# Kernel optimization log

Hardware: AMD Instinct MI355X
Metric: run time of the kernel (lower is better)

Reference implementation:

```python
import jax, jax.numpy as jnp
import numpy as np

N, E, F_IN, HID, G = 20000, 320000, 128, 128, 64
H, D = 8, 32  # TransformerConv heads, per-head dim


def setup_inputs() -> dict:
    key = jax.random.key(0)
    ks = jax.random.split(key, 24)
    def w(k, i, o):
        return (jax.random.normal(k, (i, o), jnp.float32) / np.float32(np.sqrt(i)))
    def b(k, o):
        return jax.random.normal(k, (o,), jnp.float32) * 0.01
    inp = {
        'x': jax.random.normal(ks[0], (N, F_IN), jnp.float32),
        'edge_index': jax.random.randint(ks[1], (2, E), 0, N, jnp.int32),
        'batch': jnp.sort(jax.random.randint(ks[2], (N,), 0, G, jnp.int32)),
        # SAGEConv 1: 128 -> 128 (lin_l has bias, lin_r none)
        's1_wl': w(ks[3], 128, 128), 's1_bl': b(ks[4], 128), 's1_wr': w(ks[5], 128, 128),
        # SAGEConv 2: 128 -> 256
        's2_wl': w(ks[6], 128, 256), 's2_bl': b(ks[7], 256), 's2_wr': w(ks[8], 128, 256),
        # TransformerConv 1: 256 -> 8*32
        't1_wq': w(ks[9], 256, 256), 't1_bq': b(ks[10], 256),
        't1_wk': w(ks[11], 256, 256), 't1_bk': b(ks[12], 256),
        't1_wv': w(ks[13], 256, 256), 't1_bv': b(ks[14], 256),
        't1_ws': w(ks[15], 256, 256), 't1_bs': b(ks[16], 256),
        # TransformerConv 2
        't2_wq': w(ks[17], 256, 256), 't2_bq': b(ks[18], 256),
        't2_wk': w(ks[19], 256, 256), 't2_bk': b(ks[20], 256),
        't2_wv': w(ks[21], 256, 256), 't2_bv': b(ks[22], 256),
        't2_ws': w(ks[23], 256, 256), 't2_bs': b(jax.random.fold_in(key, 100), 256),
        # proj MLP: 256 -> 512 -> HID
        'p1_w': w(jax.random.fold_in(key, 101), 256, 512), 'p1_b': b(jax.random.fold_in(key, 102), 512),
        'p2_w': w(jax.random.fold_in(key, 103), 512, HID), 'p2_b': b(jax.random.fold_in(key, 104), HID),
    }
    return inp


def _sage(x, src, dst, wl, bl, wr):
    # PyG SAGEConv (aggr='mean'): lin_l(mean_j x_j) + lin_r(x_i)
    s = jax.ops.segment_sum(x[src], dst, num_segments=N)           # [N,F]
    cnt = jax.ops.segment_sum(jnp.ones((src.shape[0], 1), x.dtype), dst, num_segments=N)
    mean = s / jnp.maximum(cnt, 1.0)
    return mean @ wl + bl + x @ wr


def _tconv(x, src, dst, wq, bq, wk, bk, wv, bv, ws, bs):
    # PyG TransformerConv(256, 32, heads=8): per-edge attention + skip
    q = (x @ wq + bq).reshape(N, H, D)
    k = (x @ wk + bk).reshape(N, H, D)
    v = (x @ wv + bv).reshape(N, H, D)
    logits = jnp.einsum('ehd,ehd->eh', q[dst], k[src]) / np.float32(np.sqrt(D))  # [E,H]
    m = jax.ops.segment_max(logits, dst, num_segments=N)           # [N,H]
    p = jnp.exp(logits - m[dst])
    denom = jax.ops.segment_sum(p, dst, num_segments=N)
    p = p / denom[dst]                                              # softmax per target node per head
    agg = jax.ops.segment_sum(p[:, :, None] * v[src], dst, num_segments=N)  # [N,H,D]
    return agg.reshape(N, H * D) + x @ ws + bs


def reference(x, edge_index, batch, s1_wl, s1_bl, s1_wr, s2_wl, s2_bl, s2_wr,
              t1_wq, t1_bq, t1_wk, t1_bk, t1_wv, t1_bv, t1_ws, t1_bs,
              t2_wq, t2_bq, t2_wk, t2_bk, t2_wv, t2_bv, t2_ws, t2_bs,
              p1_w, p1_b, p2_w, p2_b):
    src, dst = edge_index[0], edge_index[1]
    h = jax.nn.relu(_sage(x, src, dst, s1_wl, s1_bl, s1_wr))
    h = jax.nn.relu(_sage(h, src, dst, s2_wl, s2_bl, s2_wr))
    h = jax.nn.relu(_tconv(h, src, dst, t1_wq, t1_bq, t1_wk, t1_bk, t1_wv, t1_bv, t1_ws, t1_bs))
    h = jax.nn.relu(_tconv(h, src, dst, t2_wq, t2_bq, t2_wk, t2_bk, t2_wv, t2_bv, t2_ws, t2_bs))
    # proj: ReLU -> Linear(256,512) -> ReLU -> Linear(512,HID) -> Sigmoid
    h = jax.nn.relu(h)
    h = jax.nn.relu(h @ p1_w + p1_b)
    h = jax.nn.sigmoid(h @ p2_w + p2_b)
    return jax.ops.segment_max(h, batch, num_segments=G)            # global_max_pool [G,HID]
```

## Files before the change

### kernel.cpp

```cpp
#include <hip/hip_runtime.h>
#include <hip/hip_bf16.h>
#include <hip/hip_fp16.h>
#include <math.h>

#define NN 20000
#define EE 320000
#define GG 64
#define CH 16

typedef __hip_bfloat16 bf16;
typedef __attribute__((ext_vector_type(8))) short short8;
typedef __attribute__((ext_vector_type(4))) float f32x4;
typedef __attribute__((ext_vector_type(4))) uint uint4v;
typedef __attribute__((ext_vector_type(2))) _Float16 half2v;
typedef unsigned int uint;
typedef unsigned short ushort;

__device__ __forceinline__ float bfr2f(ushort u) {
    union { uint i; float f; } c; c.i = ((uint)u) << 16; return c.f;
}
__device__ __forceinline__ ushort f2bfr(float f) {
    bf16 h = __float2bfloat16(f);
    return *(ushort*)&h;
}

__device__ __forceinline__ float dot2acc(uint a, uint b, float c) {
#if __has_builtin(__builtin_amdgcn_fdot2)
    return __builtin_amdgcn_fdot2(__builtin_bit_cast(half2v, a),
                                  __builtin_bit_cast(half2v, b), c, false);
#else
    half2v ha = __builtin_bit_cast(half2v, a);
    half2v hb = __builtin_bit_cast(half2v, b);
    return c + (float)ha.x * (float)hb.x + (float)ha.y * (float)hb.y;
#endif
}

__device__ __forceinline__ void load_lds16(const void* g, void* l) {
    __builtin_amdgcn_global_load_lds(
        (const __attribute__((address_space(1))) unsigned int*)g,
        (__attribute__((address_space(3))) unsigned int*)l, 16, 0, 0);
}

template <int KW, int NW, int KTOT, int KOFF>
__device__ __forceinline__ void tpose(int local, const float* __restrict__ W,
                                      bf16* __restrict__ Wt) {
    constexpr int SH = (KW == 128) ? 7 : ((KW == 256) ? 8 : 9);
    int n = local >> SH;
    int k = local & (KW - 1);
    Wt[(size_t)n * KTOT + KOFF + k] = __float2bfloat16(W[(size_t)k * NW + n]);
}

#define PREP_CONV  10000
#define PREP_PACK  (PREP_CONV + 3200)
#define PREP_BIAS  (PREP_PACK + 8)
#define PREP_COUNT (PREP_BIAS + 1250)

__global__ __launch_bounds__(256) void prep_kernel(
    const float* x, bf16* xm1,
    const float* s1_wr, const float* s1_wl, const float* s2_wr, const float* s2_wl,
    const float* t1_wq, const float* t1_wk, const float* t1_wv, const float* t1_ws,
    const float* t2_wq, const float* t2_wk, const float* t2_wv, const float* t2_ws,
    const float* p1_w, const float* p2_w,
    bf16* w1cat, bf16* w2cat, bf16* qw1, bf16* qw2, bf16* p1t, bf16* p2t,
    const float* b1q, const float* b1k, const float* b1v, const float* b1s,
    const float* b2q, const float* b2k, const float* b2v, const float* b2s,
    float* qb1, float* qb2,
    const int* dst, int* cnt) {
    int bid = blockIdx.x;
    int tid = threadIdx.x;
    if (bid < PREP_CONV) {
        int i = bid * 256 + tid;
        int r = i >> 7, c = i & 127;
        xm1[(size_t)r * 256 + c] = __float2bfloat16(x[i]);
    } else if (bid < PREP_PACK) {
        int i = (bid - PREP_CONV) * 256 + tid;
        if (i < 16384)        tpose<128, 128, 256, 0>(i, s1_wr, w1cat);
        else if (i < 32768)   tpose<128, 128, 256, 128>(i - 16384, s1_wl, w1cat);
        else if (i < 65536)   tpose<128, 256, 256, 0>(i - 32768, s2_wr, w2cat);
        else if (i < 98304)   tpose<128, 256, 256, 128>(i - 65536, s2_wl, w2cat);
        else if (i < 163840)  tpose<256, 256, 256, 0>(i - 98304,  t1_wq, qw1);
        else if (i < 229376)  tpose<256, 256, 256, 0>(i - 163840, t1_wk, qw1 + 65536);
        else if (i < 294912)  tpose<256, 256, 256, 0>(i - 229376, t1_wv, qw1 + 131072);
        else if (i < 360448)  tpose<256, 256, 256, 0>(i - 294912, t1_ws, qw1 + 196608);
        else if (i < 425984)  tpose<256, 256, 256, 0>(i - 360448, t2_wq, qw2);
        else if (i < 491520)  tpose<256, 256, 256, 0>(i - 425984, t2_wk, qw2 + 65536);
        else if (i < 557056)  tpose<256, 256, 256, 0>(i - 491520, t2_wv, qw2 + 131072);
        else if (i < 622592)  tpose<256, 256, 256, 0>(i - 557056, t2_ws, qw2 + 196608);
        else if (i < 753664)  tpose<256, 512, 256, 0>(i - 622592, p1_w, p1t);
        else if (i < 819200)  tpose<512, 128, 512, 0>(i - 753664, p2_w, p2t);
    } else if (bid < PREP_BIAS) {
        int i = (bid - PREP_PACK) * 256 + tid;
        if (i < 2048) {
            float* d = (i < 1024) ? qb1 : qb2;
            int j = i & 1023;
            const float* s;
            if (i < 1024) s = (j < 256) ? b1q : (j < 512) ? b1k : (j < 768) ? b1v : b1s;
            else          s = (j < 256) ? b2q : (j < 512) ? b2k : (j < 768) ? b2v : b2s;
            d[j] = s[j & 255];
        }
    } else {
        int e = (bid - PREP_BIAS) * 256 + tid;
        if (e < EE) atomicAdd(&cnt[dst[e]], 1);
    }
}

__global__ __launch_bounds__(1024) void scan_kernel(int* __restrict__ cnt,
                                                    int* __restrict__ off, int n) {
    __shared__ int wsum[16];
    __shared__ int carry_s;
    int tid = threadIdx.x;
    int lane = tid & 63, wid = tid >> 6;
    if (tid == 0) { carry_s = 0; off[0] = 0; }
    __syncthreads();
    for (int base = 0; base < n; base += 1024) {
        int idx = base + tid;
        int val = (idx < n) ? cnt[idx] : 0;
        int x = val;
        #pragma unroll
        for (int s = 1; s < 64; s <<= 1) {
            int y = __shfl_up(x, s, 64);
            if (lane >= s) x += y;
        }
        if (lane == 63) wsum[wid] = x;
        __syncthreads();
        if (tid == 0) {
            int c = carry_s;
            #pragma unroll
            for (int w = 0; w < 16; w++) { int t = wsum[w]; wsum[w] = c; c += t; }
            carry_s = c;
        }
        __syncthreads();
        int incl = wsum[wid] + x;
        if (idx < n) {
            off[idx + 1] = incl;
            cnt[idx] = incl - val;
        }
        __syncthreads();
    }
}

__global__ __launch_bounds__(256) void fill_kernel(const int* __restrict__ src,
                                                   const int* __restrict__ dst,
                                                   int* __restrict__ cursor,
                                                   int* __restrict__ csr_src, int E) {
    int e = blockIdx.x * 256 + threadIdx.x;
    if (e < E) {
        int p = atomicAdd(&cursor[dst[e]], 1);
        csr_src[p] = src[e];
    }
}

__global__ __launch_bounds__(256) void mean2_kernel(const bf16* __restrict__ x, int xstride,
                                                    const int* __restrict__ off,
                                                    const int* __restrict__ csr_src,
                                                    bf16* __restrict__ outp, int ostride) {
    int node = blockIdx.x * 4 + (threadIdx.x >> 6);
    int lane = threadIdx.x & 63;
    int e0 = off[node], e1 = off[node + 1];
    float s0 = 0.f, s1 = 0.f;
    int e = e0;
    for (; e + 7 < e1; e += 8) {
        uint a[8];
        #pragma unroll
        for (int j = 0; j < 8; j++) {
            int sa = csr_src[e + j];
            a[j] = *(const uint*)(x + (size_t)sa * xstride + lane * 2);
        }
        #pragma unroll
        for (int j = 0; j < 8; j++) {
            union { uint i; float f; } t;
            t.i = a[j] << 16; s0 += t.f;
            t.i = a[j] & 0xffff0000u; s1 += t.f;
        }
    }
    for (; e < e1; e++) {
        int sa = csr_src[e];
        uint a = *(const uint*)(x + (size_t)sa * xstride + lane * 2);
        union { uint i; float f; } t;
        t.i = a << 16; s0 += t.f; t.i = a & 0xffff0000u; s1 += t.f;
    }
    int deg = e1 - e0;
    float inv = (deg > 0) ? 1.f / (float)deg : 0.f;
    uint r = ((uint)f2bfr(s1 * inv) << 16) | (uint)f2bfr(s0 * inv);
    *(uint*)(outp + (size_t)node * ostride + lane * 2) = r;
}

template <int MODE, int TM>
__global__ __launch_bounds__(256, (TM == 128) ? 3 : 4)
void gemm_kernel(const bf16* __restrict__ A,
                 const bf16* __restrict__ Wt,
                 const float* __restrict__ bias,
                 void* __restrict__ Cv,
                 int M, int K, int N, int cstride,
                 const int* __restrict__ batch,
                 float* __restrict__ pool_out) {
    constexpr int NT = (TM == 128) ? 4 : 2;
    __shared__ short As[TM * 64];
    __shared__ short Bs[128 * 64];
    __shared__ int bat[TM];
    int t = threadIdx.x;
    int lane = t & 63;
    int wave = t >> 6;
    int wm = (TM == 128) ? (wave >> 1) * 64 : 0;
    int wn = (TM == 128) ? (wave & 1) * 64 : wave * 32;
    int bm = blockIdx.y * TM, bn = blockIdx.x * 128;
    int quad = lane >> 4, l16 = lane & 15;
    int srow = t >> 3;
    int scol = (t & 7) * 8;

    if (MODE == 4 && t < TM) bat[t] = batch[min(bm + t, M - 1)];

    f32x4 acc[4][NT];
    f32x4 zero = {0.f, 0.f, 0.f, 0.f};
    #pragma unroll
    for (int i = 0; i < 4; i++)
        #pragma unroll
        for (int j = 0; j < NT; j++) acc[i][j] = zero;

    for (int kk = 0; kk < K; kk += 64) {
        #pragma unroll
        for (int r = 0; r < TM / 32; r++) {
            int row = r * 32 + srow;
            int gm = bm + row; gm = (gm < M) ? gm : (M - 1);
            load_lds16(A + (size_t)gm * K + kk + scol, &As[row * 64 + scol]);
        }
        #pragma unroll
        for (int r = 0; r < 4; r++) {
            int row = r * 32 + srow;
            load_lds16(Wt + (size_t)(bn + row) * K + kk + scol, &Bs[row * 64 + scol]);
        }
        __syncthreads();
        #pragma unroll
        for (int ks = 0; ks < 2; ks++) {
            short8 af[4], bfr[NT];
            #pragma unroll
            for (int i = 0; i < 4; i++)
                af[i] = *(const short8*)&As[(wm + i * 16 + l16) * 64 + ks * 32 + quad * 8];
            #pragma unroll
            for (int j = 0; j < NT; j++)
                bfr[j] = *(const short8*)&Bs[(wn + j * 16 + l16) * 64 + ks * 32 + quad * 8];
            #pragma unroll
            for (int i = 0; i < 4; i++)
                #pragma unroll
                for (int j = 0; j < NT; j++)
                    acc[i][j] = __builtin_amdgcn_mfma_f32_16x16x32_bf16(af[i], bfr[j], acc[i][j], 0, 0, 0);
        }
        __syncthreads();
    }

    if (MODE == 4) {
        int g0 = bat[0], gL = bat[TM - 1];
        #pragma unroll
        for (int j = 0; j < NT; j++) {
            int gn = bn + wn + j * 16 + l16;
            float m0 = 0.f, m1 = 0.f;
            #pragma unroll
            for (int i = 0; i < 4; i++) {
                #pragma unroll
                for (int r = 0; r < 4; r++) {
                    int row = i * 16 + quad * 4 + r;
                    int gm = bm + row;
                    if (gm >= M) continue;
                    float v = acc[i][j][r] + bias[gn];
                    v = 1.f / (1.f + expf(-v));
                    int g = bat[row];
                    if (g == g0) m0 = fmaxf(m0, v);
                    else if (g == gL) m1 = fmaxf(m1, v);
                    else atomicMax((int*)&pool_out[g * 128 + gn], __float_as_int(v));
                }
            }
            m0 = fmaxf(m0, __shfl_xor(m0, 16));
            m0 = fmaxf(m0, __shfl_xor(m0, 32));
            m1 = fmaxf(m1, __shfl_xor(m1, 16));
            m1 = fmaxf(m1, __shfl_xor(m1, 32));
            if (quad == 0) {
                atomicMax((int*)&pool_out[g0 * 128 + gn], __float_as_int(m0));
                if (gL != g0)
                    atomicMax((int*)&pool_out[gL * 128 + gn], __float_as_int(m1));
            }
        }
        return;
    }

    #pragma unroll
    for (int i = 0; i < 4; i++) {
        int gm0 = bm + wm + i * 16 + quad * 4;
        #pragma unroll
        for (int j = 0; j < NT; j++) {
            int gn = bn + wn + j * 16 + l16;
            #pragma unroll
            for (int r = 0; r < 4; r++) {
                int gm = gm0 + r;
                if (gm >= M) continue;
                float v = acc[i][j][r] + bias[gn];
                if (MODE == 2) v = fmaxf(v, 0.f);
                ushort st;
                if (MODE == 5 && gn < 512) {
                    __half hh = __float2half(v);
                    st = *(ushort*)&hh;
                } else {
                    st = f2bfr(v);
                }
                ((ushort*)Cv)[(size_t)gm * cstride + gn] = st;
            }
        }
    }
}

template <int MODE, int TM>
static void launch_gemm(const bf16* A, const bf16* Wt, const float* bias, void* C,
                        int M, int K, int N, int cstride, hipStream_t st,
                        const int* batch = nullptr, float* pool_out = nullptr) {
    dim3 grid(N / 128, (M + TM - 1) / TM);
    hipLaunchKernelGGL((gemm_kernel<MODE, TM>), grid, dim3(256), 0, st,
                       A, Wt, bias, C, M, K, N, cstride, batch, pool_out);
}

__global__ __launch_bounds__(256) void attn5_kernel(const bf16* __restrict__ qkvs,
                                                    const int* __restrict__ off,
                                                    const int* __restrict__ csr_src,
                                                    bf16* __restrict__ out, int ostride) {
    __shared__ float pp[2][CH][9];
    __shared__ int srcs[2][CH];
    int i = blockIdx.x;
    int tid = threadIdx.x;
    int ea = tid >> 4, ha = (tid >> 1) & 7, half = tid & 1;
    int hc = tid >> 5, dp = (tid >> 1) & 15, epar = tid & 1;

    uint q2[8];
    {
        const uint4v* qp = (const uint4v*)(qkvs + (size_t)i * 1024 + ha * 32 + half * 16);
        uint4v a = qp[0], b = qp[1];
        q2[0] = a.x; q2[1] = a.y; q2[2] = a.z; q2[3] = a.w;
        q2[4] = b.x; q2[5] = b.y; q2[6] = b.z; q2[7] = b.w;
    }

    int e0 = off[i], e1 = off[i + 1];
    float l = 0.f, acc0 = 0.f, acc1 = 0.f;
    int vcol = 512 + hc * 32 + dp * 2;
    if (e0 < e1) {
        if (tid < CH) srcs[0][tid] = csr_src[min(e0 + tid, e1 - 1)];
        __syncthreads();
        int buf = 0;
        for (int base = e0; base < e1; base += CH, buf ^= 1) {
            int cnt = min(CH, e1 - base);
            uint vv[8];
            #pragma unroll
            for (int j = 0; j < 8; j++) {
                int e = epar + j * 2;
                vv[j] = *(const uint*)(qkvs + (size_t)srcs[buf][e] * 1024 + vcol);
            }
            int s = srcs[buf][ea];
            const uint4v* kp = (const uint4v*)(qkvs + (size_t)s * 1024 + 256 + ha * 32 + half * 16);
            uint4v ka = kp[0], kb = kp[1];
            if (tid < CH) srcs[buf ^ 1][tid] = csr_src[min(base + CH + tid, e1 - 1)];
            float d = 0.f;
            d = dot2acc(q2[0], ka.x, d); d = dot2acc(q2[1], ka.y, d);
            d = dot2acc(q2[2], ka.z, d); d = dot2acc(q2[3], ka.w, d);
            d = dot2acc(q2[4], kb.x, d); d = dot2acc(q2[5], kb.y, d);
            d = dot2acc(q2[6], kb.z, d); d = dot2acc(q2[7], kb.w, d);
            d += __shfl_xor(d, 1);
            float p = (ea < cnt) ? __expf(d * 0.17677669529663687f) : 0.f;
            if (half == 0) pp[buf][ea][ha] = p;
            __syncthreads();
            #pragma unroll
            for (int j = 0; j < 8; j++) {
                int e = epar + j * 2;
                float pj = pp[buf][e][hc];
                l += pj;
                union { uint i; float f; } lo, hi;
                lo.i = vv[j] << 16; hi.i = vv[j] & 0xffff0000u;
                acc0 += pj * lo.f;
                acc1 += pj * hi.f;
            }
        }
    }
    acc0 += __shfl_xor(acc0, 1);
    acc1 += __shfl_xor(acc1, 1);
    l    += __shfl_xor(l, 1);
    float inv = (l > 0.f) ? 1.f / l : 0.f;
    float r0 = acc0 * inv, r1 = acc1 * inv;
    if (epar == 0) {
        uint su = *(const uint*)(qkvs + (size_t)i * 1024 + 768 + hc * 32 + dp * 2);
        union { uint i; float f; } lo, hi;
        lo.i = su << 16; hi.i = su & 0xffff0000u;
        float v0 = fmaxf(r0 + lo.f, 0.f);
        float v1 = fmaxf(r1 + hi.f, 0.f);
        uint packed = ((uint)f2bfr(v1) << 16) | (uint)f2bfr(v0);
        *(uint*)(out + (size_t)i * ostride + hc * 32 + dp * 2) = packed;
    }
}

extern "C" void kernel_launch(void* const* d_in, const int* in_sizes, int n_in,
                              void* d_out, int out_size, void* d_ws, size_t ws_size,
                              hipStream_t stream) {
    const float* x      = (const float*)d_in[0];
    const int*   ei     = (const int*)d_in[1];
    const int*   batch  = (const int*)d_in[2];
    const float* s1_wl  = (const float*)d_in[3];
    const float* s1_bl  = (const float*)d_in[4];
    const float* s1_wr  = (const float*)d_in[5];
    const float* s2_wl  = (const float*)d_in[6];
    const float* s2_bl  = (const float*)d_in[7];
    const float* s2_wr  = (const float*)d_in[8];
    const float* t1_wq  = (const float*)d_in[9];
    const float* t1_bq  = (const float*)d_in[10];
    const float* t1_wk  = (const float*)d_in[11];
    const float* t1_bk  = (const float*)d_in[12];
    const float* t1_wv  = (const float*)d_in[13];
    const float* t1_bv  = (const float*)d_in[14];
    const float* t1_ws  = (const float*)d_in[15];
    const float* t1_bs  = (const float*)d_in[16];
    const float* t2_wq  = (const float*)d_in[17];
    const float* t2_bq  = (const float*)d_in[18];
    const float* t2_wk  = (const float*)d_in[19];
    const float* t2_bk  = (const float*)d_in[20];
    const float* t2_wv  = (const float*)d_in[21];
    const float* t2_bv  = (const float*)d_in[22];
    const float* t2_wsk = (const float*)d_in[23];
    const float* t2_bs  = (const float*)d_in[24];
    const float* p1_w   = (const float*)d_in[25];
    const float* p1_b   = (const float*)d_in[26];
    const float* p2_w   = (const float*)d_in[27];
    const float* p2_b   = (const float*)d_in[28];
    float* out = (float*)d_out;

    char* ws = (char*)d_ws;
    size_t o = 0;
    auto alloc = [&](size_t bytes) { char* p = ws + o; o += (bytes + 255) & ~(size_t)255; return p; };
    int* off     = (int*)alloc(sizeof(int) * (NN + 1));
    int* cursor  = (int*)alloc(sizeof(int) * NN);
    int* csr_src = (int*)alloc(sizeof(int) * EE);
    bf16* w1cat = (bf16*)alloc(2 * 128 * 256);
    bf16* w2cat = (bf16*)alloc(2 * 256 * 256);
    bf16* qw1   = (bf16*)alloc(2 * 1024 * 256);
    bf16* qw2   = (bf16*)alloc(2 * 1024 * 256);
    bf16* p1t   = (bf16*)alloc(2 * 512 * 256);
    bf16* p2t   = (bf16*)alloc(2 * 128 * 512);
    float* qb1  = (float*)alloc(4 * 1024);
    float* qb2  = (float*)alloc(4 * 1024);
    bf16* xm1   = (bf16*)alloc(2 * (size_t)NN * 256);
    bf16* xm2   = (bf16*)alloc(2 * (size_t)NN * 256);
    bf16* t1b   = (bf16*)alloc(2 * (size_t)NN * 512);
    bf16* Q     = (bf16*)alloc(2 * (size_t)NN * 1024);
    bf16* h2   = xm1;
    bf16* t1   = t1b;
    bf16* h4   = xm1;
    bf16* p1o  = t1b;

    const int* src = ei;
    const int* dst = ei + EE;

    hipMemsetAsync(cursor, 0, sizeof(int) * NN, stream);
    hipMemsetAsync(out, 0, sizeof(float) * (size_t)out_size, stream);

    prep_kernel<<<PREP_COUNT, 256, 0, stream>>>(
        x, xm1,
        s1_wr, s1_wl, s2_wr, s2_wl,
        t1_wq, t1_wk, t1_wv, t1_ws,
        t2_wq, t2_wk, t2_wv, t2_wsk,
        p1_w, p2_w,
        w1cat, w2cat, qw1, qw2, p1t, p2t,
        t1_bq, t1_bk, t1_bv, t1_bs,
        t2_bq, t2_bk, t2_bv, t2_bs,
        qb1, qb2,
        dst, cursor);

    scan_kernel<<<1, 1024, 0, stream>>>(cursor, off, NN);
    fill_kernel<<<(EE + 255) / 256, 256, 0, stream>>>(src, dst, cursor, csr_src, EE);

    mean2_kernel<<<NN / 4, 256, 0, stream>>>(xm1, 256, off, csr_src, xm1 + 128, 256);
    launch_gemm<2, 64>(xm1, w1cat, s1_bl, xm2, NN, 256, 128, 256, stream);

    mean2_kernel<<<NN / 4, 256, 0, stream>>>(xm2, 256, off, csr_src, xm2 + 128, 256);
    launch_gemm<2, 64>(xm2, w2cat, s2_bl, h2, NN, 256, 256, 256, stream);

    launch_gemm<5, 128>(h2, qw1, qb1, Q, NN, 256, 1024, 1024, stream);
    attn5_kernel<<<NN, 256, 0, stream>>>(Q, off, csr_src, t1, 256);

    launch_gemm<5, 128>(t1, qw2, qb2, Q, NN, 256, 1024, 1024, stream);
    attn5_kernel<<<NN, 256, 0, stream>>>(Q, off, csr_src, h4, 256);

    launch_gemm<2, 128>(h4, p1t, p1_b, p1o, NN, 256, 512, 512, stream);
    launch_gemm<4, 64>(p1o, p2t, p2_b, nullptr, NN, 512, 128, 128, stream, batch, out);
}
```

Baseline: 437.5 us.

## Map one wavefront per node in attention and drop shared-memory syncs

```diff
diff --git a/kernel.cpp b/kernel.cpp
--- a/kernel.cpp
+++ b/kernel.cpp
@@ -6,12 +6,12 @@
 #define NN 20000
 #define EE 320000
 #define GG 64
-#define CH 16
 
 typedef __hip_bfloat16 bf16;
 typedef __attribute__((ext_vector_type(8))) short short8;
 typedef __attribute__((ext_vector_type(4))) float f32x4;
-typedef __attribute__((ext_vector_type(4))) uint uint4v;
+typedef __attribute__((ext_vector_type(4))) unsigned int uint4v;
+typedef __attribute__((ext_vector_type(2))) unsigned int uint2v;
 typedef __attribute__((ext_vector_type(2))) _Float16 half2v;
 typedef unsigned int uint;
 typedef unsigned short ushort;
@@ -316,79 +316,76 @@
                        A, Wt, bias, C, M, K, N, cstride, batch, pool_out);
 }
 
-__global__ __launch_bounds__(256) void attn5_kernel(const bf16* __restrict__ qkvs,
-                                                    const int* __restrict__ off,
-                                                    const int* __restrict__ csr_src,
-                                                    bf16* __restrict__ out, int ostride) {
-    __shared__ float pp[2][CH][9];
-    __shared__ int srcs[2][CH];
-    int i = blockIdx.x;
+__global__ __launch_bounds__(256, 8) void attn6_kernel(const bf16* __restrict__ qkvs,
+                                                       const int* __restrict__ off,
+                                                       const int* __restrict__ csr_src,
+                                                       bf16* __restrict__ out, int ostride) {
     int tid = threadIdx.x;
-    int ea = tid >> 4, ha = (tid >> 1) & 7, half = tid & 1;
-    int hc = tid >> 5, dp = (tid >> 1) & 15, epar = tid & 1;
-
-    uint q2[8];
-    {
-        const uint4v* qp = (const uint4v*)(qkvs + (size_t)i * 1024 + ha * 32 + half * 16);
-        uint4v a = qp[0], b = qp[1];
-        q2[0] = a.x; q2[1] = a.y; q2[2] = a.z; q2[3] = a.w;
-        q2[4] = b.x; q2[5] = b.y; q2[6] = b.z; q2[7] = b.w;
-    }
-
-    int e0 = off[i], e1 = off[i + 1];
-    float l = 0.f, acc0 = 0.f, acc1 = 0.f;
-    int vcol = 512 + hc * 32 + dp * 2;
+    int node = blockIdx.x * 4 + (tid >> 6);
+    int l = tid & 63;
+    int g = l >> 4;
+    int lg = l & 15;
+    int h = l >> 3;
+
+    const bf16* row_i = qkvs + (size_t)node * 1024;
+    uint4v qa = *(const uint4v*)(row_i + lg * 16);
+    uint4v qb = *(const uint4v*)(row_i + lg * 16 + 8);
+
+    int e0 = off[node], e1 = off[node + 1];
+    float acc0 = 0.f, acc1 = 0.f, acc2 = 0.f, acc3 = 0.f, lsum = 0.f;
+
     if (e0 < e1) {
-        if (tid < CH) srcs[0][tid] = csr_src[min(e0 + tid, e1 - 1)];
-        __syncthreads();
-        int buf = 0;
-        for (int base = e0; base < e1; base += CH, buf ^= 1) {
-            int cnt = min(CH, e1 - base);
-            uint vv[8];
-            #pragma unroll
-            for (int j = 0; j < 8; j++) {
-                int e = epar + j * 2;
-                vv[j] = *(const uint*)(qkvs + (size_t)srcs[buf][e] * 1024 + vcol);
+        int sc[4];
+        #pragma unroll
+        for (int e = 0; e < 4; e++) sc[e] = csr_src[min(e0 + e, e1 - 1)];
+        for (int base = e0; base < e1; base += 4) {
+            int cnt = e1 - base;
+            int sn[4];
+            #pragma unroll
+            for (int e = 0; e < 4; e++) sn[e] = csr_src[min(base + 4 + e, e1 - 1)];
+            const bf16* krow = qkvs + (size_t)sc[g] * 1024 + 256 + lg * 16;
+            uint4v ka = *(const uint4v*)(krow);
+            uint4v kb = *(const uint4v*)(krow + 8);
+            uint2v vv[4];
+            #pragma unroll
+            for (int e = 0; e < 4; e++)
+                vv[e] = *(const uint2v*)(qkvs + (size_t)sc[e] * 1024 + 512 + 4 * l);
+            float d = 0.f;
+            d = dot2acc(qa.x, ka.x, d); d = dot2acc(qa.y, ka.y, d);
+            d = dot2acc(qa.z, ka.z, d); d = dot2acc(qa.w, ka.w, d);
+            d = dot2acc(qb.x, kb.x, d); d = dot2acc(qb.y, kb.y, d);
+            d = dot2acc(qb.z, kb.z, d); d = dot2acc(qb.w, kb.w, d);
+            d += __shfl_xor(d, 1);
+            float p = (g < cnt) ? __expf(d * 0.17677669529663687f) : 0.f;
+            #pragma unroll
+            for (int e = 0; e < 4; e++) {
+                float pe = __shfl(p, e * 16 + h * 2);
+                lsum += pe;
+                union { uint i; float f; } c0, c1, c2, c3;
+                c0.i = vv[e].x << 16; c1.i = vv[e].x & 0xffff0000u;
+                c2.i = vv[e].y << 16; c3.i = vv[e].y & 0xffff0000u;
+                acc0 += pe * c0.f;
+                acc1 += pe * c1.f;
+                acc2 += pe * c2.f;
+                acc3 += pe * c3.f;
             }
-            int s = srcs[buf][ea];
-            const uint4v* kp = (const uint4v*)(qkvs + (size_t)s * 1024 + 256 + ha * 32 + half * 16);
-            uint4v ka = kp[0], kb = kp[1];
-            if (tid < CH) srcs[buf ^ 1][tid] = csr_src[min(base + CH + tid, e1 - 1)];
-            float d = 0.f;
-            d = dot2acc(q2[0], ka.x, d); d = dot2acc(q2[1], ka.y, d);
-            d = dot2acc(q2[2], ka.z, d); d = dot2acc(q2[3], ka.w, d);
-            d = dot2acc(q2[4], kb.x, d); d = dot2acc(q2[5], kb.y, d);
-            d = dot2acc(q2[6], kb.z, d); d = dot2acc(q2[7], kb.w, d);
-            d += __shfl_xor(d, 1);
-            float p = (ea < cnt) ? __expf(d * 0.17677669529663687f) : 0.f;
-            if (half == 0) pp[buf][ea][ha] = p;
-            __syncthreads();
-            #pragma unroll
-            for (int j = 0; j < 8; j++) {
-                int e = epar + j * 2;
-                float pj = pp[buf][e][hc];
-                l += pj;
-                union { uint i; float f; } lo, hi;
-                lo.i = vv[j] << 16; hi.i = vv[j] & 0xffff0000u;
-                acc0 += pj * lo.f;
-                acc1 += pj * hi.f;
-            }
-        }
-    }
-    acc0 += __shfl_xor(acc0, 1);
-    acc1 += __shfl_xor(acc1, 1);
-    l    += __shfl_xor(l, 1);
-    float inv = (l > 0.f) ? 1.f / l : 0.f;
-    float r0 = acc0 * inv, r1 = acc1 * inv;
-    if (epar == 0) {
-        uint su = *(const uint*)(qkvs + (size_t)i * 1024 + 768 + hc * 32 + dp * 2);
-        union { uint i; float f; } lo, hi;
-        lo.i = su << 16; hi.i = su & 0xffff0000u;
-        float v0 = fmaxf(r0 + lo.f, 0.f);
-        float v1 = fmaxf(r1 + hi.f, 0.f);
-        uint packed = ((uint)f2bfr(v1) << 16) | (uint)f2bfr(v0);
-        *(uint*)(out + (size_t)i * ostride + hc * 32 + dp * 2) = packed;
-    }
+            #pragma unroll
+            for (int e = 0; e < 4; e++) sc[e] = sn[e];
+        }
+    }
+    float inv = (lsum > 0.f) ? 1.f / lsum : 0.f;
+    uint2v su = *(const uint2v*)(row_i + 768 + 4 * l);
+    union { uint i; float f; } s0, s1, s2, s3;
+    s0.i = su.x << 16; s1.i = su.x & 0xffff0000u;
+    s2.i = su.y << 16; s3.i = su.y & 0xffff0000u;
+    float r0 = fmaxf(acc0 * inv + s0.f, 0.f);
+    float r1 = fmaxf(acc1 * inv + s1.f, 0.f);
+    float r2 = fmaxf(acc2 * inv + s2.f, 0.f);
+    float r3 = fmaxf(acc3 * inv + s3.f, 0.f);
+    uint2v packed;
+    packed.x = ((uint)f2bfr(r1) << 16) | (uint)f2bfr(r0);
+    packed.y = ((uint)f2bfr(r3) << 16) | (uint)f2bfr(r2);
+    *(uint2v*)(out + (size_t)node * ostride + 4 * l) = packed;
 }
 
 extern "C" void kernel_launch(void* const* d_in, const int* in_sizes, int n_in,
@@ -476,10 +473,10 @@
     launch_gemm<2, 64>(xm2, w2cat, s2_bl, h2, NN, 256, 256, 256, stream);
 
     launch_gemm<5, 128>(h2, qw1, qb1, Q, NN, 256, 1024, 1024, stream);
-    attn5_kernel<<<NN, 256, 0, stream>>>(Q, off, csr_src, t1, 256);
+    attn6_kernel<<<NN / 4, 256, 0, stream>>>(Q, off, csr_src, t1, 256);
 
     launch_gemm<5, 128>(t1, qw2, qb2, Q, NN, 256, 1024, 1024, stream);
-    attn5_kernel<<<NN, 256, 0, stream>>>(Q, off, csr_src, h4, 256);
+    attn6_kernel<<<NN / 4, 256, 0, stream>>>(Q, off, csr_src, h4, 256);
 
     launch_gemm<2, 128>(h4, p1t, p1_b, p1o, NN, 256, 512, 512, stream);
     launch_gemm<4, 64>(p1o, p2t, p2_b, nullptr, NN, 512, 128, 128, stream, batch, out);
```

After: 446.6 us. +2.1%, slower.
